# Kernel optimization log

Hardware: AMD Instinct MI355X
Metric: run time of the kernel (lower is better)

Reference implementation:

```python
import jax, jax.numpy as jnp
import numpy as np
from jax import lax

RATIOS = (0.5, 1.0, 2.0)
SCALES = (8, 16, 32)
BASE = 16
STRIDE = 16
NMS_THRESH = 0.7
N_PRE = 6000   # n_test_pre_nms
N_POST = 300   # n_test_post_nms
MIN_SIZE = 16.0  # min_size * scale (scale=1.0)
NEG = -1e9


def _anchor_base():
    py = px = BASE / 2.0
    ab = np.zeros((len(RATIOS) * len(SCALES), 4), np.float32)
    for i, r in enumerate(RATIOS):
        for j, s in enumerate(SCALES):
            h = BASE * s * np.sqrt(r)
            w = BASE * s * np.sqrt(1.0 / r)
            k = i * len(SCALES) + j
            ab[k] = [py - h / 2.0, px - w / 2.0, py + h / 2.0, px + w / 2.0]
    return ab


def _anchors(hh, ww):
    # enumerate shifted anchors, shape [hh*ww*9, 4] in (y1,x1,y2,x2)
    ab = _anchor_base()
    sy = np.arange(hh, dtype=np.float32) * STRIDE
    sx = np.arange(ww, dtype=np.float32) * STRIDE
    sx, sy = np.meshgrid(sx, sy)
    shift = np.stack([sy.ravel(), sx.ravel(), sy.ravel(), sx.ravel()], axis=1)
    a = (ab[None, :, :] + shift[:, None, :]).reshape(-1, 4).astype(np.float32)
    return jnp.asarray(a)


def _conv(x, w, b, pad):
    y = lax.conv_general_dilated(x, w, (1, 1), [(pad, pad), (pad, pad)],
                                 dimension_numbers=('NCHW', 'OIHW', 'NCHW'))
    return y + b[None, :, None, None]


def _nms(boxes, valid):
    # greedy NMS over score-sorted boxes [N,4]; returns N_POST selected indices (-1 = pad)
    N = boxes.shape[0]
    y1, x1, y2, x2 = boxes[:, 0], boxes[:, 1], boxes[:, 2], boxes[:, 3]
    area = (y2 - y1) * (x2 - x1)
    idx = jnp.arange(N)

    def body(i, sup):
        cur = valid[i] & (~sup[i])
        ih = jnp.clip(jnp.minimum(y2[i], y2) - jnp.maximum(y1[i], y1), 0.0)
        iw = jnp.clip(jnp.minimum(x2[i], x2) - jnp.maximum(x1[i], x1), 0.0)
        inter = ih * iw
        iou = inter / (area[i] + area - inter + 1e-9)
        return sup | (cur & (iou > NMS_THRESH) & (idx > i))

    sup = lax.fori_loop(0, N, body, jnp.zeros((N,), bool))
    kept = valid & (~sup)
    rank = jnp.cumsum(kept) - 1
    sel = jnp.full((N_POST,), -1, jnp.int32)
    sel = sel.at[jnp.where(kept & (rank < N_POST), rank, N_POST)].set(
        jnp.arange(N, dtype=jnp.int32), mode='drop')
    return sel


def setup_inputs() -> dict:
    key = jax.random.key(0)
    ks = jax.random.split(key, 5)
    n, c, hh, ww = 8, 512, 64, 64
    x = jax.random.normal(ks[0], (n, c, hh, ww), jnp.float32)
    # normal_init(mean=0, std=0.01), biases zero
    w1 = 0.01 * jax.random.normal(ks[1], (512, 512, 3, 3), jnp.float32)
    b1 = jnp.zeros((512,), jnp.float32)
    w_score = 0.01 * jax.random.normal(ks[2], (18, 512, 1, 1), jnp.float32)
    b_score = jnp.zeros((18,), jnp.float32)
    w_loc = 0.01 * jax.random.normal(ks[3], (36, 512, 1, 1), jnp.float32)
    b_loc = jnp.zeros((36,), jnp.float32)
    return {"x": x, "w1": w1, "b1": b1, "w_score": w_score, "b_score": b_score,
            "w_loc": w_loc, "b_loc": b_loc, "img_h": 1024, "img_w": 1024}


def reference(x, w1, b1, w_score, b_score, w_loc, b_loc, img_h, img_w):
    n, _, hh, ww = x.shape
    anchor = _anchors(hh, ww)  # [K,4]
    mid = jax.nn.relu(_conv(x, w1, b1, 1))
    rpn_locs = _conv(mid, w_loc, b_loc, 0).transpose(0, 2, 3, 1).reshape(n, -1, 4)  # [n,K,4]
    raw = _conv(mid, w_score, b_score, 0).transpose(0, 2, 3, 1)  # [n,hh,ww,18]
    sm = jax.nn.softmax(raw.reshape(n, hh, ww, -1, 2), axis=-1)
    fg = sm[..., 1].reshape(n, -1)          # [n,K] foreground scores
    rpn_scores = raw.reshape(n, -1, 2)      # pre-softmax, as in original
    # loc2bbox decode
    ah = anchor[:, 2] - anchor[:, 0]
    aw = anchor[:, 3] - anchor[:, 1]
    acy = anchor[:, 0] + 0.5 * ah
    acx = anchor[:, 1] + 0.5 * aw
    dy, dx, dh, dw = (rpn_locs[..., 0], rpn_locs[..., 1], rpn_locs[..., 2], rpn_locs[..., 3])
    cy = dy * ah + acy
    cx = dx * aw + acx
    h = ah * jnp.exp(dh)
    w = aw * jnp.exp(dw)
    fh = jnp.float32(img_h)
    fw = jnp.float32(img_w)
    roi = jnp.stack([jnp.clip(cy - 0.5 * h, 0.0, fh), jnp.clip(cx - 0.5 * w, 0.0, fw),
                     jnp.clip(cy + 0.5 * h, 0.0, fh), jnp.clip(cx + 0.5 * w, 0.0, fw)], axis=-1)
    hs = roi[..., 2] - roi[..., 0]
    ws = roi[..., 3] - roi[..., 1]
    ok = (hs >= MIN_SIZE) & (ws >= MIN_SIZE)
    masked = jnp.where(ok, fg, NEG)
    vals, top = lax.top_k(masked, N_PRE)  # score-descending pre-NMS selection
    boxes = jnp.take_along_axis(roi, top[..., None], axis=1)  # [n,N_PRE,4]
    valid = vals > NEG / 2
    sel = jax.vmap(_nms)(boxes, valid)  # [n,N_POST]
    mask = sel >= 0
    rois = jnp.take_along_axis(boxes, jnp.clip(sel, 0)[..., None], axis=1)
    rois = jnp.where(mask[..., None], rois, 0.0)  # [n,N_POST,4], zero-padded
    roi_indices = jnp.where(mask, jnp.arange(n, dtype=jnp.int32)[:, None], -1)  # -1 = pad
    return (rpn_locs, rpn_scores, rois, roi_indices, anchor)
```

## Files before the change

kernel.cpp:

```cpp
#include <hip/hip_runtime.h>
#include <cstdint>
#include <cstddef>

#define CIN 512
#define NA 36864
#define NPRE 6000
#define NPOST 300
#define NARR 8192
#define NWORD 94
#define NEGV -1000000000.0f
#define ISTRIDE 76

#define O_LOCS   0
#define O_SCORES 1179648
#define O_ROIS   1769472
#define O_RIDX   1779072
#define O_ANCH   1781472

__device__ __forceinline__ float fmulr(float a, float b) { return __fmul_rn(a, b); }
__device__ __forceinline__ float faddr(float a, float b) { return __fadd_rn(a, b); }
__device__ __forceinline__ float fsubr(float a, float b) { return __fsub_rn(a, b); }

__device__ __forceinline__ void anchor_for(int a, int pos, float* anc) {
    const double rat[3] = {0.5, 1.0, 2.0};
    const double scl[3] = {8.0, 16.0, 32.0};
    int ri = a / 3, si = a - ri * 3;
    double h = 16.0 * scl[si] * sqrt(rat[ri]);
    double w = 16.0 * scl[si] * sqrt(1.0 / rat[ri]);
    float a0 = (float)(8.0 - h * 0.5);
    float a1 = (float)(8.0 - w * 0.5);
    float a2 = (float)(8.0 + h * 0.5);
    float a3 = (float)(8.0 + w * 0.5);
    int y = pos >> 6, x = pos & 63;
    float sy = (float)(y * 16), sx = (float)(x * 16);
    anc[0] = faddr(a0, sy); anc[1] = faddr(a1, sx);
    anc[2] = faddr(a2, sy); anc[3] = faddr(a3, sx);
}

__device__ __forceinline__ bool decode_box(float4 L, const float* anc, float* box) {
    float ah  = fsubr(anc[2], anc[0]);
    float aw  = fsubr(anc[3], anc[1]);
    float acy = faddr(anc[0], fmulr(0.5f, ah));
    float acx = faddr(anc[1], fmulr(0.5f, aw));
    float cy  = faddr(fmulr(L.x, ah), acy);
    float cx  = faddr(fmulr(L.y, aw), acx);
    float h   = fmulr(ah, expf(L.z));
    float w   = fmulr(aw, expf(L.w));
    float y1 = fminf(fmaxf(fsubr(cy, fmulr(0.5f, h)), 0.0f), 1024.0f);
    float x1 = fminf(fmaxf(fsubr(cx, fmulr(0.5f, w)), 0.0f), 1024.0f);
    float y2 = fminf(fmaxf(faddr(cy, fmulr(0.5f, h)), 0.0f), 1024.0f);
    float x2 = fminf(fmaxf(faddr(cx, fmulr(0.5f, w)), 0.0f), 1024.0f);
    box[0] = y1; box[1] = x1; box[2] = y2; box[3] = x2;
    float hs = fsubr(y2, y1), ws2 = fsubr(x2, x1);
    return (hs >= 16.0f) && (ws2 >= 16.0f);
}

__device__ __forceinline__ unsigned long long mono64(double f) {
    unsigned long long u = (unsigned long long)__double_as_longlong(f);
    return (u & 0x8000000000000000ull) ? ~u : (u | 0x8000000000000000ull);
}

__global__ __launch_bounds__(256) void k_wreord(const float* __restrict__ w1,
                                                float* __restrict__ wr2) {
    __shared__ float tile[64][37];
    const int ct0 = blockIdx.x * 36;
    const int ocb = blockIdx.y;
    const int t = threadIdx.x;
    for (int i = t; i < 64 * 36; i += 256) {
        int orow = i / 36, c = i - orow * 36;
        tile[orow][c] = w1[(size_t)(ocb * 64 + orow) * 4608 + ct0 + c];
    }
    __syncthreads();
    for (int i = t; i < 36 * 64; i += 256) {
        int ct = i >> 6, o = i & 63;
        wr2[((size_t)ocb * 4608 + ct0 + ct) * 64 + o] = tile[o][ct];
    }
}

__global__ __launch_bounds__(256, 2) void k_conv3(const float* __restrict__ x,
                                                  const float* __restrict__ wr2,
                                                  const float* __restrict__ b1,
                                                  float* __restrict__ mid) {
    __shared__ float in_s[8 * 6 * ISTRIDE];
    __shared__ float w_s[8 * 9 * 64];
    const int yb  = blockIdx.x;
    const int ocb = blockIdx.y;
    const int n   = blockIdx.z;
    const int t   = threadIdx.x;
    const int y0  = yb * 4;
    const int tocg = t >> 5;
    const int tx   = t & 31;
    const int r    = tx >> 3;
    const int xo   = (tx & 7) << 3;

    for (int i = t; i < 48 * 8; i += 256) {
        int row = i >> 3, c = i & 7;
        int xi = (c < 4) ? c : 64 + c;
        in_s[row * ISTRIDE + xi] = 0.f;
    }

    int   ilds[3];
    int   ival[3];
    const float* igp[3];
#pragma unroll
    for (int k = 0; k < 3; ++k) {
        int s = t + k * 256;
        int row = s >> 4, col = s & 15;
        int cc = row / 6, rr = row - cc * 6;
        int gy = y0 - 1 + rr;
        ival[k] = (gy >= 0 && gy < 64) ? 1 : 0;
        int gyc = min(max(gy, 0), 63);
        ilds[k] = row * ISTRIDE + 4 + col * 4;
        igp[k]  = x + (((size_t)(n * CIN + cc) * 64 + gyc) * 64 + col * 4);
    }
    const float* wgp = wr2 + (size_t)ocb * (4608 * 64);

    float acc[8][8];
#pragma unroll
    for (int i = 0; i < 8; i++)
#pragma unroll
        for (int j = 0; j < 8; j++) acc[i][j] = 0.f;

    for (int ch = 0; ch < 64; ++ch) {
        const float* wp0 = wgp + (size_t)ch * 4608;
#pragma unroll
        for (int k = 0; k < 4; ++k)
            *(float4*)&w_s[4 * t + 1024 * k] = *(const float4*)(wp0 + 4 * t + 1024 * k);
        if (t < 128)
            *(float4*)&w_s[4 * t + 4096] = *(const float4*)(wp0 + 4 * t + 4096);
#pragma unroll
        for (int k = 0; k < 3; ++k) {
            float4 v = make_float4(0.f, 0.f, 0.f, 0.f);
            if (ival[k]) v = *(const float4*)(igp[k] + (size_t)ch * 32768);
            *(float4*)&in_s[ilds[k]] = v;
        }
        __syncthreads();

        float sub[8][8];
#pragma unroll
        for (int i = 0; i < 8; i++)
#pragma unroll
            for (int j = 0; j < 8; j++) sub[i][j] = 0.f;
#pragma unroll 1
        for (int cc = 0; cc < 8; ++cc) {
#pragma unroll
            for (int dy = 0; dy < 3; ++dy) {
                const float4* ip =
                    (const float4*)&in_s[cc * (6 * ISTRIDE) + (r + dy) * ISTRIDE + xo];
                float4 Q0 = ip[0], Q1 = ip[1], Q2 = ip[2], Q3 = ip[3];
                float in16[16] = {Q0.x, Q0.y, Q0.z, Q0.w, Q1.x, Q1.y, Q1.z, Q1.w,
                                  Q2.x, Q2.y, Q2.z, Q2.w, Q3.x, Q3.y, Q3.z, Q3.w};
#pragma unroll
                for (int dx = 0; dx < 3; ++dx) {
                    const float4* wp =
                        (const float4*)&w_s[cc * 576 + (dy * 3 + dx) * 64 + tocg * 8];
                    float4 W0 = wp[0], W1 = wp[1];
                    float w8[8] = {W0.x, W0.y, W0.z, W0.w, W1.x, W1.y, W1.z, W1.w};
#pragma unroll
                    for (int i = 0; i < 8; i++)
#pragma unroll
                        for (int j = 0; j < 8; j++)
                            sub[i][j] += w8[i] * in16[j + dx + 3];
                }
            }
        }
#pragma unroll
        for (int i = 0; i < 8; i++)
#pragma unroll
            for (int j = 0; j < 8; j++) acc[i][j] += sub[i][j];
        __syncthreads();
    }
    const int ocbase = (ocb << 6) + tocg * 8;
#pragma unroll
    for (int i = 0; i < 8; i++) {
        float bb = b1[ocbase + i];
#pragma unroll
        for (int j = 0; j < 8; j++) {
            float v = fmaxf(acc[i][j] + bb, 0.f);
            mid[((n * CIN + ocbase + i) * 64 + (y0 + r)) * 64 + xo + j] = v;
        }
    }
}

__global__ __launch_bounds__(256) void k_conv1(const float* __restrict__ mid,
                                               const float* __restrict__ wl,
                                               const float* __restrict__ bl,
                                               const float* __restrict__ wsc,
                                               const float* __restrict__ bs,
                                               float* __restrict__ out,
                                               double* __restrict__ fgbuf) {
    __shared__ float in_s[128 * 64];
    __shared__ float w_s[54 * 128];
    const int y = blockIdx.x;
    const int n = blockIdx.y;
    const int t = threadIdx.x;
    const int xx = t & 63, og = t >> 6;
    double accd[14];
#pragma unroll
    for (int k = 0; k < 14; k++) accd[k] = 0.0;

    for (int c0 = 0; c0 < 512; c0 += 128) {
        for (int idx = t; idx < 128 * 64; idx += 256) {
            int cc = idx >> 6, x2 = idx & 63;
            in_s[idx] = mid[((n * CIN + c0 + cc) * 64 + y) * 64 + x2];
        }
        for (int idx = t; idx < 54 * 128; idx += 256) {
            int oc = idx >> 7, cc = idx & 127;
            w_s[idx] = (oc < 36) ? wl[oc * 512 + c0 + cc] : wsc[(oc - 36) * 512 + c0 + cc];
        }
        __syncthreads();
#pragma unroll 1
        for (int cc = 0; cc < 128; ++cc) {
            double iv = (double)in_s[cc * 64 + xx];
#pragma unroll
            for (int k = 0; k < 14; k++) {
                int oc = og * 14 + k;
                if (oc < 54) accd[k] += (double)w_s[oc * 128 + cc] * iv;
            }
        }
        __syncthreads();
    }
    const int pos = y * 64 + xx;
    double sv[14];
#pragma unroll
    for (int k = 0; k < 14; k++) {
        int oc = og * 14 + k;
        if (oc >= 54) break;
        if (oc < 36) {
            double v = accd[k] + (double)bl[oc];
            int a = oc >> 2, cd = oc & 3;
            out[O_LOCS + ((size_t)(n * NA + pos * 9 + a)) * 4 + cd] = (float)v;
        } else {
            sv[k] = accd[k] + (double)bs[oc - 36];
            int c2 = oc - 36, a = c2 >> 1, cls = c2 & 1;
            out[O_SCORES + ((size_t)(n * NA + pos * 9 + a)) * 2 + cls] = (float)sv[k];
        }
    }
#pragma unroll
    for (int k = 0; k < 13; k++) {
        int oc = og * 14 + k;
        if (oc >= 36 && oc < 54 && ((oc - 36) & 1) == 0) {
            double s0 = sv[k], s1 = sv[k + 1];
            double m = fmax(s0, s1);
            double e0 = exp(s0 - m), e1 = exp(s1 - m);
            double fg = e1 / (e0 + e1);
            int a = (oc - 36) >> 1;
            fgbuf[(size_t)n * NA + pos * 9 + a] = fg;
        }
    }
}

__global__ __launch_bounds__(256) void k_keys(const float* __restrict__ out_ro,
                                              const double* __restrict__ fgbuf,
                                              unsigned long long* __restrict__ keys,
                                              float* __restrict__ out) {
    const int n = blockIdx.x / 144;
    const int i = (blockIdx.x % 144) * 256 + threadIdx.x;
    int pos = i / 9, a = i - pos * 9;
    float anc[4]; anchor_for(a, pos, anc);
    float4 L = *(const float4*)&out_ro[O_LOCS + (size_t)(n * NA + i) * 4];
    float box[4];
    bool ok = decode_box(L, anc, box);
    double f = ok ? fgbuf[(size_t)n * NA + i] : (double)NEGV;
    unsigned long long m = mono64(f);
    keys[(size_t)n * NA + i] =
        (m & 0xFFFFFFFFFFFF0000ull) | (unsigned long long)(0xFFFFu - (unsigned)i);
    if (blockIdx.x < 144) {
        out[O_ANCH + (size_t)i * 4 + 0] = anc[0];
        out[O_ANCH + (size_t)i * 4 + 1] = anc[1];
        out[O_ANCH + (size_t)i * 4 + 2] = anc[2];
        out[O_ANCH + (size_t)i * 4 + 3] = anc[3];
    }
}

__global__ __launch_bounds__(1024) void k_topk(const unsigned long long* __restrict__ keys,
                                               const float* __restrict__ out,
                                               unsigned int* __restrict__ cntg,
                                               float* __restrict__ bsort,
                                               unsigned char* __restrict__ vflag) {
    __shared__ union SM {
        unsigned int hist[16384];
        unsigned long long arr[NARR];
    } sm;
    const int n = blockIdx.x, t = threadIdx.x;
    unsigned int* hist = sm.hist;
    unsigned int* gs = sm.hist + 8192;
    unsigned long long* prefp = (unsigned long long*)&sm.hist[8452];
    if (t == 0) { hist[8448] = NPRE; *prefp = 0ull; }
    __syncthreads();
    const int shifts[5] = {51, 38, 25, 12, 0};
    const int widths[5] = {13, 13, 13, 13, 12};
    int plen = 0;
    for (int lev = 0; lev < 5; ++lev) {
        const int nb = 1 << widths[lev];
        const int gsz = nb >> 8;
        for (int b = t; b < nb; b += 1024) hist[b] = 0;
        __syncthreads();
        const unsigned long long pref = *prefp;
        for (int i = t; i < NA; i += 1024) {
            unsigned long long key = keys[(size_t)n * NA + i];
            if (plen == 0 || (key >> (64 - plen)) == pref) {
                unsigned int bin = (unsigned int)((key >> shifts[lev]) & (unsigned)(nb - 1));
                atomicAdd(&hist[bin], 1u);
            }
        }
        __syncthreads();
        if (t < 256) {
            unsigned int s = 0;
            for (int m = 0; m < gsz; m++) s += hist[t * gsz + m];
            gs[t] = s;
        }
        __syncthreads();
        for (int off = 1; off < 256; off <<= 1) {
            unsigned int v = 0;
            if (t < 256 && t + off < 256) v = gs[t + off];
            __syncthreads();
            if (t < 256) gs[t] += v;
            __syncthreads();
        }
        const unsigned int rem = hist[8448];
        if (t < 256) {
            unsigned int here = gs[t];
            unsigned int above = (t == 255) ? 0u : gs[t + 1];
            if (here >= rem && above < rem) hist[8449] = (unsigned int)t;
        }
        __syncthreads();
        if (t == 0) {
            int G = (int)hist[8449];
            unsigned int acc = (G == 255) ? 0u : gs[G + 1];
            int selbin = G * gsz;
            for (int b = G * gsz + gsz - 1; b >= G * gsz; --b) {
                if (acc + hist[b] >= rem) { selbin = b; break; }
                acc += hist[b];
            }
            hist[8448] = rem - acc;
            *prefp = ((*prefp) << widths[lev]) | (unsigned long long)(unsigned)selbin;
        }
        plen += widths[lev];
        __syncthreads();
    }
    const unsigned long long kth = *prefp;
    if (t == 0) cntg[n] = 0u;
    __syncthreads();
    unsigned long long* arr = sm.arr;
    for (int i = t; i < NA; i += 1024) {
        unsigned long long key = keys[(size_t)n * NA + i];
        if (key >= kth) {
            unsigned int p = atomicAdd(&cntg[n], 1u);
            if (p < NARR) arr[p] = key;
        }
    }
    __syncthreads();
    for (int idx = NPRE + t; idx < NARR; idx += 1024) arr[idx] = 0ull;
    __syncthreads();
    for (int k = 2; k <= NARR; k <<= 1)
        for (int j = k >> 1; j > 0; j >>= 1) {
            for (int i = t; i < NARR; i += 1024) {
                int ixj = i ^ j;
                if (ixj > i) {
                    unsigned long long a = arr[i], b = arr[ixj];
                    bool up = (i & k) == 0;
                    if (up ? (a < b) : (a > b)) { arr[i] = b; arr[ixj] = a; }
                }
            }
            __syncthreads();
        }
    for (int r = t; r < NPRE; r += 1024) {
        unsigned long long key = arr[r];
        unsigned int i = 0xFFFFu - (unsigned int)(key & 0xFFFFull);
        int pos = i / 9, a = i - pos * 9;
        float anc[4]; anchor_for(a, pos, anc);
        float4 L = *(const float4*)&out[O_LOCS + (size_t)(n * NA + i) * 4];
        float box[4];
        bool ok = decode_box(L, anc, box);
        ((float4*)bsort)[(size_t)n * NPRE + r] = make_float4(box[0], box[1], box[2], box[3]);
        vflag[(size_t)n * NPRE + r] = ok ? 1 : 0;
    }
}

__global__ __launch_bounds__(256) void k_mask(const float* __restrict__ bsort,
                                              unsigned long long* __restrict__ masks) {
    __shared__ float4 bx[1024];
    const int n  = blockIdx.z;
    const int jc = blockIdx.y;
    const int i  = blockIdx.x * 256 + threadIdx.x;
    const bool have = i < NPRE;
    float4 bi = make_float4(0, 0, 0, 0); float areai = 0.f;
    if (have) {
        bi = ((const float4*)bsort)[(size_t)n * NPRE + i];
        areai = fmulr(fsubr(bi.z, bi.x), fsubr(bi.w, bi.y));
    }
    const int jn = min(1024, NPRE - jc * 1024);
    for (int jj = threadIdx.x; jj < jn; jj += 256)
        bx[jj] = ((const float4*)bsort)[(size_t)n * NPRE + jc * 1024 + jj];
    __syncthreads();
    for (int w = 0; w < 16; ++w) {
        int gw = jc * 16 + w;
        if (gw >= NWORD) break;
        unsigned long long m = 0ull;
        int jbase = jc * 1024 + w * 64;
        if (have && jbase + 63 > i) {
#pragma unroll 1
            for (int b = 0; b < 64; b++) {
                int j = jbase + b;
                if (j > i && j < NPRE) {
                    float4 bj = bx[w * 64 + b];
                    float ih = fmaxf(fsubr(fminf(bi.z, bj.z), fmaxf(bi.x, bj.x)), 0.f);
                    float iw = fmaxf(fsubr(fminf(bi.w, bj.w), fmaxf(bi.y, bj.y)), 0.f);
                    float inter = fmulr(ih, iw);
                    float areaj = fmulr(fsubr(bj.z, bj.x), fsubr(bj.w, bj.y));
                    float den = faddr(fsubr(faddr(areai, areaj), inter), 1e-9f);
                    float iou = __fdiv_rn(inter, den);
                    if (iou > 0.7f) m |= (1ull << b);
                }
            }
        }
        if (have) masks[((size_t)n * NPRE + i) * NWORD + gw] = m;
    }
}

__global__ __launch_bounds__(64) void k_scan(const unsigned long long* __restrict__ masks,
                                             const unsigned char* __restrict__ vflag,
                                             const float* __restrict__ bsort,
                                             float* __restrict__ out) {
    const int n = blockIdx.x;
    const int l = threadIdx.x;
    unsigned long long valw0 = 0ull, valw1 = 0ull;
    for (int w = 0; w < NWORD; ++w) {
        int idx = w * 64 + l;
        bool v = (idx < NPRE) && (vflag[(size_t)n * NPRE + idx] != 0);
        unsigned long long word = __ballot(v);
        if (w == l) valw0 = word;
        if (w == 64 + l) valw1 = word;
    }
    unsigned long long sup0 = 0ull, sup1 = 0ull;
    int kept = 0;
    while (kept < NPOST) {
        unsigned long long cand0 = valw0 & ~sup0;
        unsigned long long cand1 = (l < NWORD - 64) ? (valw1 & ~sup1) : 0ull;
        unsigned long long b0 = __ballot(cand0 != 0ull);
        int w; unsigned long long bits;
        if (b0) {
            int fl = __ffsll((long long)b0) - 1;
            w = fl; bits = __shfl(cand0, fl);
        } else {
            unsigned long long b1 = __ballot(cand1 != 0ull);
            if (!b1) break;
            int fl = __ffsll((long long)b1) - 1;
            w = 64 + fl; bits = __shfl(cand1, fl);
        }
        int i = w * 64 + (__ffsll((long long)bits) - 1);
        if (l == 0) {
            float4 b4 = ((const float4*)bsort)[(size_t)n * NPRE + i];
            out[O_ROIS + (size_t)(n * NPOST + kept) * 4 + 0] = b4.x;
            out[O_ROIS + (size_t)(n * NPOST + kept) * 4 + 1] = b4.y;
            out[O_ROIS + (size_t)(n * NPOST + kept) * 4 + 2] = b4.z;
            out[O_ROIS + (size_t)(n * NPOST + kept) * 4 + 3] = b4.w;
            out[O_RIDX + n * NPOST + kept] = (float)n;
        }
        kept++;
        if (kept >= NPOST) break;
        const unsigned long long* mrow = masks + ((size_t)n * NPRE + i) * NWORD;
        sup0 |= mrow[l];
        if (l < NWORD - 64) sup1 |= mrow[64 + l];
        if (w < 64) { if (l == w) sup0 |= (1ull << (i & 63)); }
        else        { if (l == w - 64) sup1 |= (1ull << (i & 63)); }
    }
    for (int r = kept + l; r < NPOST; r += 64) {
        out[O_ROIS + (size_t)(n * NPOST + r) * 4 + 0] = 0.f;
        out[O_ROIS + (size_t)(n * NPOST + r) * 4 + 1] = 0.f;
        out[O_ROIS + (size_t)(n * NPOST + r) * 4 + 2] = 0.f;
        out[O_ROIS + (size_t)(n * NPOST + r) * 4 + 3] = 0.f;
        out[O_RIDX + n * NPOST + r] = -1.0f;
    }
}

extern "C" void kernel_launch(void* const* d_in, const int* in_sizes, int n_in,
                              void* d_out, int out_size, void* d_ws, size_t ws_size,
                              hipStream_t stream) {
    const float* x   = (const float*)d_in[0];
    const float* w1  = (const float*)d_in[1];
    const float* b1  = (const float*)d_in[2];
    const float* wsc = (const float*)d_in[3];
    const float* bsc = (const float*)d_in[4];
    const float* wlc = (const float*)d_in[5];
    const float* blc = (const float*)d_in[6];
    float* out = (float*)d_out;
    char* ws = (char*)d_ws;

    float* wr2                = (float*)(ws + 0);
    float* mid                = (float*)(ws + 9437184);
    double* fgbuf             = (double*)(ws + 76546048);
    unsigned long long* keys  = (unsigned long long*)(ws + 78905344);
    unsigned int* cntg        = (unsigned int*)(ws + 81265152);
    float* bsort              = (float*)(ws + 81789952);
    unsigned char* vflag      = (unsigned char*)(ws + 82557952);
    unsigned long long* masks = (unsigned long long*)(ws + 82606080);

    dim3 gw(128, 8);
    k_wreord<<<gw, 256, 0, stream>>>(w1, wr2);
    dim3 g3(16, 8, 8);
    k_conv3<<<g3, 256, 0, stream>>>(x, wr2, b1, mid);
    dim3 g1(64, 8);
    k_conv1<<<g1, 256, 0, stream>>>(mid, wlc, blc, wsc, bsc, out, fgbuf);
    k_keys<<<1152, 256, 0, stream>>>(out, fgbuf, keys, out);
    k_topk<<<8, 1024, 0, stream>>>(keys, out, cntg, bsort, vflag);
    dim3 gm(24, 6, 8);
    k_mask<<<gm, 256, 0, stream>>>(bsort, masks);
    k_scan<<<8, 64, 0, stream>>>(masks, vflag, bsort, out);
}
```

Before: 3.002 ms.

## Split top-k into select/compact/rank kernels; widen conv3 channel chunk; vectorize conv1 weights

The single-block-per-image top-k, which ended in an 8192-element bitonic sort, is split into three kernels: a radix select of the k-th key, a grid-wide compaction, and a rank-by-counting kernel that places each box directly at its sorted position. This spreads the sort over many blocks instead of one per image. The 3x3 conv now stages 16 input channels per shared-memory load rather than 8, halving barriers but doubling LDS use. The 1x1 conv weights are rearranged in shared memory so each thread reads them with float4 loads. Rank by counting assumes the keys are unique.

```diff
diff --git a/kernel.cpp b/kernel.cpp
--- a/kernel.cpp
+++ b/kernel.cpp
@@ -6,7 +6,6 @@
 #define NA 36864
 #define NPRE 6000
 #define NPOST 300
-#define NARR 8192
 #define NWORD 94
 #define NEGV -1000000000.0f
 #define ISTRIDE 76
@@ -81,8 +80,8 @@
                                                   const float* __restrict__ wr2,
                                                   const float* __restrict__ b1,
                                                   float* __restrict__ mid) {
-    __shared__ float in_s[8 * 6 * ISTRIDE];
-    __shared__ float w_s[8 * 9 * 64];
+    __shared__ float in_s[16 * 6 * ISTRIDE];
+    __shared__ float w_s[16 * 9 * 64];
     const int yb  = blockIdx.x;
     const int ocb = blockIdx.y;
     const int n   = blockIdx.z;
@@ -93,17 +92,17 @@
     const int r    = tx >> 3;
     const int xo   = (tx & 7) << 3;
 
-    for (int i = t; i < 48 * 8; i += 256) {
+    for (int i = t; i < 96 * 8; i += 256) {
         int row = i >> 3, c = i & 7;
         int xi = (c < 4) ? c : 64 + c;
         in_s[row * ISTRIDE + xi] = 0.f;
     }
 
-    int   ilds[3];
-    int   ival[3];
-    const float* igp[3];
-#pragma unroll
-    for (int k = 0; k < 3; ++k) {
+    int   ilds[6];
+    int   ival[6];
+    const float* igp[6];
+#pragma unroll
+    for (int k = 0; k < 6; ++k) {
         int s = t + k * 256;
         int row = s >> 4, col = s & 15;
         int cc = row / 6, rr = row - cc * 6;
@@ -121,53 +120,55 @@
 #pragma unroll
         for (int j = 0; j < 8; j++) acc[i][j] = 0.f;
 
-    for (int ch = 0; ch < 64; ++ch) {
-        const float* wp0 = wgp + (size_t)ch * 4608;
-#pragma unroll
-        for (int k = 0; k < 4; ++k)
+    for (int ch = 0; ch < 32; ++ch) {
+        const float* wp0 = wgp + (size_t)ch * 9216;
+#pragma unroll
+        for (int k = 0; k < 9; ++k)
             *(float4*)&w_s[4 * t + 1024 * k] = *(const float4*)(wp0 + 4 * t + 1024 * k);
-        if (t < 128)
-            *(float4*)&w_s[4 * t + 4096] = *(const float4*)(wp0 + 4 * t + 4096);
-#pragma unroll
-        for (int k = 0; k < 3; ++k) {
+#pragma unroll
+        for (int k = 0; k < 6; ++k) {
             float4 v = make_float4(0.f, 0.f, 0.f, 0.f);
-            if (ival[k]) v = *(const float4*)(igp[k] + (size_t)ch * 32768);
+            if (ival[k]) v = *(const float4*)(igp[k] + (size_t)ch * 65536);
             *(float4*)&in_s[ilds[k]] = v;
         }
         __syncthreads();
 
-        float sub[8][8];
-#pragma unroll
-        for (int i = 0; i < 8; i++)
-#pragma unroll
-            for (int j = 0; j < 8; j++) sub[i][j] = 0.f;
 #pragma unroll 1
-        for (int cc = 0; cc < 8; ++cc) {
-#pragma unroll
-            for (int dy = 0; dy < 3; ++dy) {
-                const float4* ip =
-                    (const float4*)&in_s[cc * (6 * ISTRIDE) + (r + dy) * ISTRIDE + xo];
-                float4 Q0 = ip[0], Q1 = ip[1], Q2 = ip[2], Q3 = ip[3];
-                float in16[16] = {Q0.x, Q0.y, Q0.z, Q0.w, Q1.x, Q1.y, Q1.z, Q1.w,
-                                  Q2.x, Q2.y, Q2.z, Q2.w, Q3.x, Q3.y, Q3.z, Q3.w};
-#pragma unroll
-                for (int dx = 0; dx < 3; ++dx) {
-                    const float4* wp =
-                        (const float4*)&w_s[cc * 576 + (dy * 3 + dx) * 64 + tocg * 8];
-                    float4 W0 = wp[0], W1 = wp[1];
-                    float w8[8] = {W0.x, W0.y, W0.z, W0.w, W1.x, W1.y, W1.z, W1.w};
-#pragma unroll
-                    for (int i = 0; i < 8; i++)
-#pragma unroll
-                        for (int j = 0; j < 8; j++)
-                            sub[i][j] += w8[i] * in16[j + dx + 3];
+        for (int half = 0; half < 2; ++half) {
+            float sub[8][8];
+#pragma unroll
+            for (int i = 0; i < 8; i++)
+#pragma unroll
+                for (int j = 0; j < 8; j++) sub[i][j] = 0.f;
+#pragma unroll 1
+            for (int cc2 = 0; cc2 < 8; ++cc2) {
+                const int cc = half * 8 + cc2;
+#pragma unroll
+                for (int dy = 0; dy < 3; ++dy) {
+                    const float4* ip =
+                        (const float4*)&in_s[cc * (6 * ISTRIDE) + (r + dy) * ISTRIDE + xo];
+                    float4 Q0 = ip[0], Q1 = ip[1], Q2 = ip[2], Q3 = ip[3];
+                    float in16[16] = {Q0.x, Q0.y, Q0.z, Q0.w, Q1.x, Q1.y, Q1.z, Q1.w,
+                                      Q2.x, Q2.y, Q2.z, Q2.w, Q3.x, Q3.y, Q3.z, Q3.w};
+#pragma unroll
+                    for (int dx = 0; dx < 3; ++dx) {
+                        const float4* wp =
+                            (const float4*)&w_s[cc * 576 + (dy * 3 + dx) * 64 + tocg * 8];
+                        float4 W0 = wp[0], W1 = wp[1];
+                        float w8[8] = {W0.x, W0.y, W0.z, W0.w, W1.x, W1.y, W1.z, W1.w};
+#pragma unroll
+                        for (int i = 0; i < 8; i++)
+#pragma unroll
+                            for (int j = 0; j < 8; j++)
+                                sub[i][j] += w8[i] * in16[j + dx + 3];
+                    }
                 }
             }
-        }
-#pragma unroll
-        for (int i = 0; i < 8; i++)
-#pragma unroll
-            for (int j = 0; j < 8; j++) acc[i][j] += sub[i][j];
+#pragma unroll
+            for (int i = 0; i < 8; i++)
+#pragma unroll
+                for (int j = 0; j < 8; j++) acc[i][j] += sub[i][j];
+        }
         __syncthreads();
     }
     const int ocbase = (ocb << 6) + tocg * 8;
@@ -190,7 +191,7 @@
                                                float* __restrict__ out,
                                                double* __restrict__ fgbuf) {
     __shared__ float in_s[128 * 64];
-    __shared__ float w_s[54 * 128];
+    __shared__ float w_s[128 * 64];
     const int y = blockIdx.x;
     const int n = blockIdx.y;
     const int t = threadIdx.x;
@@ -204,19 +205,26 @@
             int cc = idx >> 6, x2 = idx & 63;
             in_s[idx] = mid[((n * CIN + c0 + cc) * 64 + y) * 64 + x2];
         }
-        for (int idx = t; idx < 54 * 128; idx += 256) {
-            int oc = idx >> 7, cc = idx & 127;
-            w_s[idx] = (oc < 36) ? wl[oc * 512 + c0 + cc] : wsc[(oc - 36) * 512 + c0 + cc];
+        for (int idx = t; idx < 128 * 64; idx += 256) {
+            int cc = idx >> 6, s = idx & 63;
+            int og2 = s >> 4, kk = s & 15;
+            int oc = og2 * 14 + kk;
+            float v = 0.f;
+            if (kk < 14 && oc < 54)
+                v = (oc < 36) ? wl[oc * 512 + c0 + cc] : wsc[(oc - 36) * 512 + c0 + cc];
+            w_s[cc * 64 + s] = v;
         }
         __syncthreads();
 #pragma unroll 1
         for (int cc = 0; cc < 128; ++cc) {
             double iv = (double)in_s[cc * 64 + xx];
-#pragma unroll
-            for (int k = 0; k < 14; k++) {
-                int oc = og * 14 + k;
-                if (oc < 54) accd[k] += (double)w_s[oc * 128 + cc] * iv;
-            }
+            const float4* wq = (const float4*)&w_s[cc * 64 + og * 16];
+            float4 W0 = wq[0], W1 = wq[1], W2 = wq[2], W3 = wq[3];
+            float wf[16] = {W0.x, W0.y, W0.z, W0.w, W1.x, W1.y, W1.z, W1.w,
+                            W2.x, W2.y, W2.z, W2.w, W3.x, W3.y, W3.z, W3.w};
+#pragma unroll
+            for (int k = 0; k < 14; k++)
+                accd[k] += (double)wf[k] * iv;
         }
         __syncthreads();
     }
@@ -273,20 +281,15 @@
     }
 }
 
-__global__ __launch_bounds__(1024) void k_topk(const unsigned long long* __restrict__ keys,
-                                               const float* __restrict__ out,
-                                               unsigned int* __restrict__ cntg,
-                                               float* __restrict__ bsort,
-                                               unsigned char* __restrict__ vflag) {
-    __shared__ union SM {
-        unsigned int hist[16384];
-        unsigned long long arr[NARR];
-    } sm;
+__global__ __launch_bounds__(1024) void k_select(const unsigned long long* __restrict__ keys,
+                                                 unsigned long long* __restrict__ kth,
+                                                 unsigned int* __restrict__ cnt) {
+    __shared__ unsigned int hist[8192];
+    __shared__ unsigned int gs[256];
+    __shared__ unsigned int s_rem, s_G;
+    __shared__ unsigned long long s_pref;
     const int n = blockIdx.x, t = threadIdx.x;
-    unsigned int* hist = sm.hist;
-    unsigned int* gs = sm.hist + 8192;
-    unsigned long long* prefp = (unsigned long long*)&sm.hist[8452];
-    if (t == 0) { hist[8448] = NPRE; *prefp = 0ull; }
+    if (t == 0) { s_rem = NPRE; s_pref = 0ull; }
     __syncthreads();
     const int shifts[5] = {51, 38, 25, 12, 0};
     const int widths[5] = {13, 13, 13, 13, 12};
@@ -296,7 +299,7 @@
         const int gsz = nb >> 8;
         for (int b = t; b < nb; b += 1024) hist[b] = 0;
         __syncthreads();
-        const unsigned long long pref = *prefp;
+        const unsigned long long pref = s_pref;
         for (int i = t; i < NA; i += 1024) {
             unsigned long long key = keys[(size_t)n * NA + i];
             if (plen == 0 || (key >> (64 - plen)) == pref) {
@@ -318,63 +321,85 @@
             if (t < 256) gs[t] += v;
             __syncthreads();
         }
-        const unsigned int rem = hist[8448];
+        const unsigned int rem = s_rem;
         if (t < 256) {
             unsigned int here = gs[t];
             unsigned int above = (t == 255) ? 0u : gs[t + 1];
-            if (here >= rem && above < rem) hist[8449] = (unsigned int)t;
+            if (here >= rem && above < rem) s_G = (unsigned int)t;
         }
         __syncthreads();
         if (t == 0) {
-            int G = (int)hist[8449];
+            int G = (int)s_G;
             unsigned int acc = (G == 255) ? 0u : gs[G + 1];
             int selbin = G * gsz;
             for (int b = G * gsz + gsz - 1; b >= G * gsz; --b) {
                 if (acc + hist[b] >= rem) { selbin = b; break; }
                 acc += hist[b];
             }
-            hist[8448] = rem - acc;
-            *prefp = ((*prefp) << widths[lev]) | (unsigned long long)(unsigned)selbin;
+            s_rem = rem - acc;
+            s_pref = (s_pref << widths[lev]) | (unsigned long long)(unsigned)selbin;
         }
         plen += widths[lev];
         __syncthreads();
     }
-    const unsigned long long kth = *prefp;
-    if (t == 0) cntg[n] = 0u;
-    __syncthreads();
-    unsigned long long* arr = sm.arr;
-    for (int i = t; i < NA; i += 1024) {
-        unsigned long long key = keys[(size_t)n * NA + i];
-        if (key >= kth) {
-            unsigned int p = atomicAdd(&cntg[n], 1u);
-            if (p < NARR) arr[p] = key;
-        }
-    }
-    __syncthreads();
-    for (int idx = NPRE + t; idx < NARR; idx += 1024) arr[idx] = 0ull;
-    __syncthreads();
-    for (int k = 2; k <= NARR; k <<= 1)
-        for (int j = k >> 1; j > 0; j >>= 1) {
-            for (int i = t; i < NARR; i += 1024) {
-                int ixj = i ^ j;
-                if (ixj > i) {
-                    unsigned long long a = arr[i], b = arr[ixj];
-                    bool up = (i & k) == 0;
-                    if (up ? (a < b) : (a > b)) { arr[i] = b; arr[ixj] = a; }
-                }
-            }
-            __syncthreads();
-        }
-    for (int r = t; r < NPRE; r += 1024) {
-        unsigned long long key = arr[r];
+    if (t == 0) { kth[n] = s_pref; cnt[n] = 0u; }
+}
+
+__global__ void k_compact(const unsigned long long* __restrict__ keys,
+                          const unsigned long long* __restrict__ kth,
+                          unsigned long long* __restrict__ cbuf,
+                          unsigned int* __restrict__ cnt) {
+    const int n = blockIdx.x / 144;
+    const int i = (blockIdx.x % 144) * 256 + threadIdx.x;
+    unsigned long long key = keys[(size_t)n * NA + i];
+    if (key >= kth[n]) {
+        unsigned int p = atomicAdd(&cnt[n], 1u);
+        if (p < 8192) cbuf[(size_t)n * 8192 + p] = key;
+    }
+}
+
+__global__ __launch_bounds__(256) void k_rank(const unsigned long long* __restrict__ cbuf,
+                                              const float* __restrict__ out,
+                                              float* __restrict__ bsort,
+                                              unsigned char* __restrict__ vflag) {
+    __shared__ unsigned long long tile[2048];
+    const int n = blockIdx.y, t = threadIdx.x;
+    const int base = blockIdx.x * 512;
+    unsigned long long mykey[2]; int myrank[2]; bool have[2];
+#pragma unroll
+    for (int m = 0; m < 2; ++m) {
+        int idx = base + t * 2 + m;
+        have[m] = idx < NPRE;
+        mykey[m] = have[m] ? cbuf[(size_t)n * 8192 + idx] : 0ull;
+        myrank[m] = 0;
+    }
+    for (int tb = 0; tb < 3; ++tb) {
+        for (int jj = t; jj < 2048; jj += 256) {
+            int j = tb * 2048 + jj;
+            tile[jj] = (j < NPRE) ? cbuf[(size_t)n * 8192 + j] : 0ull;
+        }
+        __syncthreads();
+        const int jmax = min(2048, NPRE - tb * 2048);
+        for (int j = 0; j < jmax; ++j) {
+            unsigned long long kj = tile[j];
+            if (kj > mykey[0]) myrank[0]++;
+            if (kj > mykey[1]) myrank[1]++;
+        }
+        __syncthreads();
+    }
+#pragma unroll
+    for (int m = 0; m < 2; ++m) {
+        if (!have[m]) continue;
+        unsigned long long key = mykey[m];
         unsigned int i = 0xFFFFu - (unsigned int)(key & 0xFFFFull);
         int pos = i / 9, a = i - pos * 9;
         float anc[4]; anchor_for(a, pos, anc);
         float4 L = *(const float4*)&out[O_LOCS + (size_t)(n * NA + i) * 4];
         float box[4];
         bool ok = decode_box(L, anc, box);
-        ((float4*)bsort)[(size_t)n * NPRE + r] = make_float4(box[0], box[1], box[2], box[3]);
-        vflag[(size_t)n * NPRE + r] = ok ? 1 : 0;
+        ((float4*)bsort)[(size_t)n * NPRE + myrank[m]] =
+            make_float4(box[0], box[1], box[2], box[3]);
+        vflag[(size_t)n * NPRE + myrank[m]] = ok ? 1 : 0;
     }
 }
 
@@ -492,7 +517,9 @@
     float* mid                = (float*)(ws + 9437184);
     double* fgbuf             = (double*)(ws + 76546048);
     unsigned long long* keys  = (unsigned long long*)(ws + 78905344);
-    unsigned int* cntg        = (unsigned int*)(ws + 81265152);
+    unsigned long long* kth   = (unsigned long long*)(ws + 81264640);
+    unsigned int* cnt         = (unsigned int*)(ws + 81265152);
+    unsigned long long* cbuf  = (unsigned long long*)(ws + 81265664);
     float* bsort              = (float*)(ws + 81789952);
     unsigned char* vflag      = (unsigned char*)(ws + 82557952);
     unsigned long long* masks = (unsigned long long*)(ws + 82606080);
@@ -504,7 +531,10 @@
     dim3 g1(64, 8);
     k_conv1<<<g1, 256, 0, stream>>>(mid, wlc, blc, wsc, bsc, out, fgbuf);
     k_keys<<<1152, 256, 0, stream>>>(out, fgbuf, keys, out);
-    k_topk<<<8, 1024, 0, stream>>>(keys, out, cntg, bsort, vflag);
+    k_select<<<8, 1024, 0, stream>>>(keys, kth, cnt);
+    k_compact<<<1152, 256, 0, stream>>>(keys, kth, cbuf, cnt);
+    dim3 gr(12, 8);
+    k_rank<<<gr, 256, 0, stream>>>(cbuf, out, bsort, vflag);
     dim3 gm(24, 6, 8);
     k_mask<<<gm, 256, 0, stream>>>(bsort, masks);
     k_scan<<<8, 64, 0, stream>>>(masks, vflag, bsort, out);
```

New measurement: 2.793 ms. -7.0%, faster.
